# Kernel optimization log

Hardware: AMD Instinct MI355X
Metric: run time of the kernel (lower is better)

Reference implementation:

```python
import jax, jax.numpy as jnp
import numpy as np

N_NODES = 50000
N_EDGES = 1200000
D_FEAT = 64
HIDDEN = 32


def setup_inputs() -> dict:
    key = jax.random.key(0)
    ks = jax.random.split(key, 9)
    x = jax.random.normal(ks[0], (N_NODES, D_FEAT), dtype=jnp.float32)
    edge_index = jax.random.randint(ks[1], (2, N_EDGES), 0, N_NODES, dtype=jnp.int64)
    u = jax.random.normal(ks[2], (N_NODES,), dtype=jnp.float32)
    d_in = 2 * D_FEAT
    # MLP: Linear(d_in,H) -> relu -> Linear(H,H) -> relu -> Linear(H,1)
    W1 = jax.random.normal(ks[3], (d_in, HIDDEN), dtype=jnp.float32) / np.sqrt(d_in)
    b1 = jnp.zeros((HIDDEN,), dtype=jnp.float32)
    W2 = jax.random.normal(ks[4], (HIDDEN, HIDDEN), dtype=jnp.float32) / np.sqrt(HIDDEN)
    b2 = jnp.zeros((HIDDEN,), dtype=jnp.float32)
    W3 = jax.random.normal(ks[5], (HIDDEN, 1), dtype=jnp.float32) / np.sqrt(HIDDEN)
    b3 = jnp.zeros((1,), dtype=jnp.float32)
    return {"x": x, "edge_index": edge_index, "u": u,
            "W1": W1, "b1": b1, "W2": W2, "b2": b2, "W3": W3, "b3": b3}


def reference(x, edge_index, u, W1, b1, W2, b2, W3, b3):
    row, col = edge_index[0], edge_index[1]
    # gather + concat: [E, 2*D]
    x_edge = jnp.concatenate([x[row], x[col]], axis=-1)
    # per-edge MLP -> scalar weight per edge
    h = jax.nn.relu(x_edge @ W1 + b1)
    h = jax.nn.relu(h @ W2 + b2)
    edge_weight = (h @ W3 + b3)[:, 0]  # [E]
    # spmm: f[i] = sum_{e: row[e]==i} w_e * u[col[e]]
    f = jax.ops.segment_sum(edge_weight * u[col], row, num_segments=x.shape[0])
    return f
```

## Files before the change

kernel.cpp:

```cpp
#include <hip/hip_runtime.h>

#define N_NODES 50000
#define N_EDGES 1200000
#define N_TILES (N_NODES / 16)
#define W1T_STRIDE 72
#define K1_BLOCKS 782

#define N_BUCKETS 196
#define BUCKET_CAP 7168
#define CHUNKS_PER_WAVE 15
#define EDGES_PER_BLOCK 1920
#define KA_BLOCKS 625

typedef __attribute__((ext_vector_type(8))) short short8;
typedef __attribute__((ext_vector_type(4))) float floatx4;

__device__ __forceinline__ unsigned short f32_to_bf16(float f) {
    unsigned int v = __float_as_uint(f);
    unsigned int r = v + 0x7FFFu + ((v >> 16) & 1u);
    return (unsigned short)(r >> 16);
}
__device__ __forceinline__ float bf16_to_f32(unsigned short s) {
    return __uint_as_float(((unsigned int)s) << 16);
}
__device__ __forceinline__ unsigned int pack_bf16x2(float lo, float hi) {
    return (unsigned int)f32_to_bf16(lo) | ((unsigned int)f32_to_bf16(hi) << 16);
}

__global__ __launch_bounds__(256) void precompute_P_mfma(
    const float* __restrict__ x, const float* __restrict__ W1,
    const float* __restrict__ b1, unsigned short* __restrict__ P,
    int* __restrict__ cursor)
{
    const int tid  = threadIdx.x;
    const int gtid = blockIdx.x * 256 + tid;

    if (gtid < N_BUCKETS) cursor[gtid] = 0;

    __shared__ unsigned short W1t[64 * W1T_STRIDE];
    for (int e = tid; e < 128 * 32; e += 256) {
        const int kp = e >> 5, jp = e & 31;
        W1t[((kp < 64) ? jp : jp + 32) * W1T_STRIDE + (kp & 63)] =
            f32_to_bf16(W1[e]);
    }
    __syncthreads();

    const int lane = tid & 63;
    const int n = lane & 15;
    const int q = lane >> 4;

    const int tile = blockIdx.x * 4 + (tid >> 6);
    if (tile >= N_TILES) return;

    short8 bw[4][2];
    #pragma unroll
    for (int G = 0; G < 4; ++G)
        #pragma unroll
        for (int h = 0; h < 2; ++h)
            bw[G][h] = *(const short8*)
                &W1t[(n + 16 * G) * W1T_STRIDE + h * 32 + q * 8];
    const float bias0 = b1[n], bias1 = b1[n + 16];

    const int node = tile * 16 + n;
    const float4* xp  = (const float4*)(x + (size_t)node * 64 + q * 8);
    const float4 xa = xp[0], xb = xp[1];
    const float4* xp2 = (const float4*)(x + (size_t)node * 64 + 32 + q * 8);
    const float4 xc = xp2[0], xd = xp2[1];

    short8 a0, a1;
    a0[0] = (short)f32_to_bf16(xa.x); a0[1] = (short)f32_to_bf16(xa.y);
    a0[2] = (short)f32_to_bf16(xa.z); a0[3] = (short)f32_to_bf16(xa.w);
    a0[4] = (short)f32_to_bf16(xb.x); a0[5] = (short)f32_to_bf16(xb.y);
    a0[6] = (short)f32_to_bf16(xb.z); a0[7] = (short)f32_to_bf16(xb.w);
    a1[0] = (short)f32_to_bf16(xc.x); a1[1] = (short)f32_to_bf16(xc.y);
    a1[2] = (short)f32_to_bf16(xc.z); a1[3] = (short)f32_to_bf16(xc.w);
    a1[4] = (short)f32_to_bf16(xd.x); a1[5] = (short)f32_to_bf16(xd.y);
    a1[6] = (short)f32_to_bf16(xd.z); a1[7] = (short)f32_to_bf16(xd.w);

    unsigned int* P32 = (unsigned int*)P;
    floatx4 acc[4];
    #pragma unroll
    for (int G = 0; G < 4; ++G) {
        const float bi = (G == 0) ? bias0 : (G == 1) ? bias1 : 0.0f;
        acc[G] = (floatx4){bi, bi, bi, bi};
        acc[G] = __builtin_amdgcn_mfma_f32_16x16x32_bf16(a0, bw[G][0], acc[G], 0, 0, 0);
        acc[G] = __builtin_amdgcn_mfma_f32_16x16x32_bf16(a1, bw[G][1], acc[G], 0, 0, 0);
    }
    #pragma unroll
    for (int r = 0; r < 4; ++r) {
        const int nr = tile * 16 + q * 4 + r;
        P32[(size_t)nr * 32 + n]      = pack_bf16x2(acc[0][r], acc[1][r]);
        P32[(size_t)nr * 32 + 16 + n] = pack_bf16x2(acc[2][r], acc[3][r]);
    }
}

__global__ __launch_bounds__(256) void edge_mlp_bin(
    const int* __restrict__ row, const int* __restrict__ col,
    const float* __restrict__ u,
    const float* __restrict__ W2, const float* __restrict__ b2,
    const float* __restrict__ W3, const float* __restrict__ b3,
    const unsigned short* __restrict__ P,
    unsigned int* __restrict__ buf, int* __restrict__ cursor)
{
    __shared__ unsigned short rankv[EDGES_PER_BLOCK];
    __shared__ int hist[N_BUCKETS];
    __shared__ int base[N_BUCKETS];

    const int tid = threadIdx.x;
    for (int b = tid; b < N_BUCKETS; b += 256) hist[b] = 0;
    __syncthreads();

    const int blockStart = blockIdx.x * EDGES_PER_BLOCK;

    for (int i = tid; i < EDGES_PER_BLOCK; i += 256) {
        const int r = row[blockStart + i];
        rankv[i] = (unsigned short)atomicAdd(&hist[r >> 8], 1);
    }
    __syncthreads();

    for (int b = tid; b < N_BUCKETS; b += 256)
        base[b] = atomicAdd(&cursor[b], hist[b]);
    __syncthreads();

    const int lane = tid & 63;
    const int n = lane & 15;
    const int q = lane >> 4;
    const int wave = tid >> 6;

    short8 bf0, bf1;
    #pragma unroll
    for (int i = 0; i < 8; ++i) {
        const int F = q * 4 + (i >> 1) + 16 * (i & 1);
        bf0[i] = (short)f32_to_bf16(W2[F * 32 + n]);
        bf1[i] = (short)f32_to_bf16(W2[F * 32 + n + 16]);
    }
    const float w3n0 = W3[n], w3n1 = W3[n + 16];
    const float b2n0 = b2[n], b2n1 = b2[n + 16];
    const float bias3 = b3[0];

    #pragma unroll 1
    for (int ci = 0; ci < CHUNKS_PER_WAVE; ++ci) {
        const int cloc  = (wave * CHUNKS_PER_WAVE + ci) * 32;
        const int base0 = blockStart + cloc;

        int rI[2], cI[2];
        #pragma unroll
        for (int t = 0; t < 2; ++t) {
            const int e = base0 + t * 16 + n;
            rI[t] = row[e];
            cI[t] = col[e];
        }
        int r2 = 0, eloc = 0; float u2 = 0.0f;
        if (n < 8) {
            eloc = cloc + 16 * (n >> 2) + 4 * q + (n & 3);
            const int e2 = blockStart + eloc;
            r2 = row[e2];
            u2 = u[col[e2]];
        }
        short8 v1[2], v2[2];
        #pragma unroll
        for (int t = 0; t < 2; ++t) {
            v1[t] = *(const short8*)(P + (size_t)rI[t] * 64 + q * 8);
            v2[t] = *(const short8*)(P + (size_t)cI[t] * 64 + 32 + q * 8);
        }

        float tr[2][4];
        #pragma unroll
        for (int t = 0; t < 2; ++t) {
            short8 a;
            #pragma unroll
            for (int i = 0; i < 8; ++i) {
                const float f1 = bf16_to_f32((unsigned short)v1[t][i]);
                const float f2 = bf16_to_f32((unsigned short)v2[t][i]);
                a[i] = (short)f32_to_bf16(fmaxf(f1 + f2, 0.0f));
            }
            floatx4 d0 = {b2n0, b2n0, b2n0, b2n0};
            floatx4 d1 = {b2n1, b2n1, b2n1, b2n1};
            d0 = __builtin_amdgcn_mfma_f32_16x16x32_bf16(a, bf0, d0, 0, 0, 0);
            d1 = __builtin_amdgcn_mfma_f32_16x16x32_bf16(a, bf1, d1, 0, 0, 0);
            #pragma unroll
            for (int r = 0; r < 4; ++r)
                tr[t][r] = fmaxf(d0[r], 0.0f) * w3n0 + fmaxf(d1[r], 0.0f) * w3n1;
        }

        #pragma unroll
        for (int mask = 1; mask < 16; mask <<= 1) {
            #pragma unroll
            for (int t = 0; t < 2; ++t)
                #pragma unroll
                for (int r = 0; r < 4; ++r)
                    tr[t][r] += __shfl_xor(tr[t][r], mask, 64);
        }

        if (n < 8) {
            const float va0 = (n & 4) ? tr[1][0] : tr[0][0];
            const float va1 = (n & 4) ? tr[1][1] : tr[0][1];
            const float va2 = (n & 4) ? tr[1][2] : tr[0][2];
            const float va3 = (n & 4) ? tr[1][3] : tr[0][3];
            const float vb0 = (n & 2) ? va2 : va0;
            const float vb1 = (n & 2) ? va3 : va1;
            const float v   = (n & 1) ? vb1 : vb0;
            const float val = (v + bias3) * u2;

            const int bin  = r2 >> 8;
            const int slot = base[bin] + (int)rankv[eloc];
            buf[(size_t)bin * BUCKET_CAP + slot] =
                ((unsigned int)f32_to_bf16(val) << 16) | (unsigned int)(r2 & 255);
        }
    }
}

__global__ __launch_bounds__(256) void bucket_reduce(
    const unsigned int* __restrict__ buf, const int* __restrict__ cursor,
    float* __restrict__ out)
{
    __shared__ float acc[256];
    const int b   = blockIdx.x;
    const int tid = threadIdx.x;
    acc[tid] = 0.0f;
    __syncthreads();

    const int cnt = cursor[b];
    const unsigned int* bb = buf + (size_t)b * BUCKET_CAP;
    for (int i = tid; i < cnt; i += 256) {
        const unsigned int ent = bb[i];
        atomicAdd(&acc[ent & 255u],
                  bf16_to_f32((unsigned short)(ent >> 16)));
    }
    __syncthreads();

    const int node = b * 256 + tid;
    if (node < N_NODES) out[node] = acc[tid];
}

extern "C" void kernel_launch(void* const* d_in, const int* in_sizes, int n_in,
                              void* d_out, int out_size, void* d_ws, size_t ws_size,
                              hipStream_t stream)
{
    const float* x    = (const float*)d_in[0];
    const int*   eidx = (const int*)  d_in[1];
    const float* u    = (const float*)d_in[2];
    const float* W1   = (const float*)d_in[3];
    const float* b1   = (const float*)d_in[4];
    const float* W2   = (const float*)d_in[5];
    const float* b2   = (const float*)d_in[6];
    const float* W3   = (const float*)d_in[7];
    const float* b3   = (const float*)d_in[8];

    const int* row = eidx;
    const int* col = eidx + N_EDGES;

    unsigned short* P   = (unsigned short*)d_ws;
    unsigned int*   buf = (unsigned int*)((char*)d_ws + (size_t)N_NODES * 128);
    int* cursor = (int*)((char*)d_ws + (size_t)N_NODES * 128
                         + (size_t)N_BUCKETS * BUCKET_CAP * 4);
    float* out = (float*)d_out;

    precompute_P_mfma<<<K1_BLOCKS, 256, 0, stream>>>(x, W1, b1, P, cursor);

    edge_mlp_bin<<<KA_BLOCKS, 256, 0, stream>>>(
        row, col, u, W2, b2, W3, b3, P, buf, cursor);

    bucket_reduce<<<N_BUCKETS, 256, 0, stream>>>(buf, cursor, out);
}
```

Baseline: 150.2 us.

## Bin edges by destination first, then run edge MLP per bucket with shared-memory accumulation

The pipeline is reordered. Edges are first binned by row bucket, storing (local row, col) entries, and a per-bucket kernel then runs the MLP and accumulates directly into LDS before atomically adding to the output. The P table is split into row and col halves so row-side gathers stay within a bucket's compact 16KB slice, which should improve cache locality. The separate reduce kernel and the bf16 rounding of edge values are gone. In exchange, the output needs zero-initialisation and global atomics, and the work per bucket is uneven.

```diff
diff --git a/kernel.cpp b/kernel.cpp
--- a/kernel.cpp
+++ b/kernel.cpp
@@ -8,9 +8,9 @@
 
 #define N_BUCKETS 196
 #define BUCKET_CAP 7168
-#define CHUNKS_PER_WAVE 15
 #define EDGES_PER_BLOCK 1920
 #define KA_BLOCKS 625
+#define KB_SPLIT 4
 
 typedef __attribute__((ext_vector_type(8))) short short8;
 typedef __attribute__((ext_vector_type(4))) float floatx4;
@@ -29,13 +29,16 @@
 
 __global__ __launch_bounds__(256) void precompute_P_mfma(
     const float* __restrict__ x, const float* __restrict__ W1,
-    const float* __restrict__ b1, unsigned short* __restrict__ P,
-    int* __restrict__ cursor)
+    const float* __restrict__ b1,
+    unsigned short* __restrict__ P1, unsigned short* __restrict__ P2,
+    int* __restrict__ cursor, float* __restrict__ out)
 {
     const int tid  = threadIdx.x;
     const int gtid = blockIdx.x * 256 + tid;
 
     if (gtid < N_BUCKETS) cursor[gtid] = 0;
+    for (int i = gtid; i < N_NODES; i += K1_BLOCKS * 256)
+        out[i] = 0.0f;
 
     __shared__ unsigned short W1t[64 * W1T_STRIDE];
     for (int e = tid; e < 128 * 32; e += 256) {
@@ -77,7 +80,6 @@
     a1[4] = (short)f32_to_bf16(xd.x); a1[5] = (short)f32_to_bf16(xd.y);
     a1[6] = (short)f32_to_bf16(xd.z); a1[7] = (short)f32_to_bf16(xd.w);
 
-    unsigned int* P32 = (unsigned int*)P;
     floatx4 acc[4];
     #pragma unroll
     for (int G = 0; G < 4; ++G) {
@@ -86,41 +88,63 @@
         acc[G] = __builtin_amdgcn_mfma_f32_16x16x32_bf16(a0, bw[G][0], acc[G], 0, 0, 0);
         acc[G] = __builtin_amdgcn_mfma_f32_16x16x32_bf16(a1, bw[G][1], acc[G], 0, 0, 0);
     }
+    unsigned int* P1d = (unsigned int*)P1;
+    unsigned int* P2d = (unsigned int*)P2;
     #pragma unroll
     for (int r = 0; r < 4; ++r) {
         const int nr = tile * 16 + q * 4 + r;
-        P32[(size_t)nr * 32 + n]      = pack_bf16x2(acc[0][r], acc[1][r]);
-        P32[(size_t)nr * 32 + 16 + n] = pack_bf16x2(acc[2][r], acc[3][r]);
-    }
-}
-
-__global__ __launch_bounds__(256) void edge_mlp_bin(
+        P1d[(size_t)nr * 16 + n] = pack_bf16x2(acc[0][r], acc[1][r]);
+        P2d[(size_t)nr * 16 + n] = pack_bf16x2(acc[2][r], acc[3][r]);
+    }
+}
+
+__global__ __launch_bounds__(256) void edge_bin(
     const int* __restrict__ row, const int* __restrict__ col,
+    unsigned int* __restrict__ buf, int* __restrict__ cursor)
+{
+    __shared__ unsigned short rankv[EDGES_PER_BLOCK];
+    __shared__ int hist[N_BUCKETS];
+    __shared__ int base[N_BUCKETS];
+
+    const int tid = threadIdx.x;
+    for (int b = tid; b < N_BUCKETS; b += 256) hist[b] = 0;
+    __syncthreads();
+
+    const int blockStart = blockIdx.x * EDGES_PER_BLOCK;
+
+    for (int i = tid; i < EDGES_PER_BLOCK; i += 256) {
+        const int r = row[blockStart + i];
+        rankv[i] = (unsigned short)atomicAdd(&hist[r >> 8], 1);
+    }
+    __syncthreads();
+
+    for (int b = tid; b < N_BUCKETS; b += 256)
+        base[b] = atomicAdd(&cursor[b], hist[b]);
+    __syncthreads();
+
+    for (int i = tid; i < EDGES_PER_BLOCK; i += 256) {
+        const int r = row[blockStart + i];
+        const int c = col[blockStart + i];
+        const int bin = r >> 8;
+        buf[(size_t)bin * BUCKET_CAP + base[bin] + (int)rankv[i]] =
+            ((unsigned int)(r & 255) << 24) | (unsigned int)c;
+    }
+}
+
+__global__ __launch_bounds__(256) void bucket_mlp(
     const float* __restrict__ u,
     const float* __restrict__ W2, const float* __restrict__ b2,
     const float* __restrict__ W3, const float* __restrict__ b3,
-    const unsigned short* __restrict__ P,
-    unsigned int* __restrict__ buf, int* __restrict__ cursor)
-{
-    __shared__ unsigned short rankv[EDGES_PER_BLOCK];
-    __shared__ int hist[N_BUCKETS];
-    __shared__ int base[N_BUCKETS];
-
+    const unsigned short* __restrict__ P1, const unsigned short* __restrict__ P2,
+    const unsigned int* __restrict__ buf, const int* __restrict__ cursor,
+    float* __restrict__ out)
+{
+    __shared__ float accs[256];
     const int tid = threadIdx.x;
-    for (int b = tid; b < N_BUCKETS; b += 256) hist[b] = 0;
-    __syncthreads();
-
-    const int blockStart = blockIdx.x * EDGES_PER_BLOCK;
-
-    for (int i = tid; i < EDGES_PER_BLOCK; i += 256) {
-        const int r = row[blockStart + i];
-        rankv[i] = (unsigned short)atomicAdd(&hist[r >> 8], 1);
-    }
-    __syncthreads();
-
-    for (int b = tid; b < N_BUCKETS; b += 256)
-        base[b] = atomicAdd(&cursor[b], hist[b]);
-    __syncthreads();
+    accs[tid] = 0.0f;
+
+    const int b = blockIdx.x >> 2;
+    const int s = blockIdx.x & (KB_SPLIT - 1);
 
     const int lane = tid & 63;
     const int n = lane & 15;
@@ -138,30 +162,38 @@
     const float b2n0 = b2[n], b2n1 = b2[n + 16];
     const float bias3 = b3[0];
 
+    __syncthreads();
+
+    const int cnt = cursor[b];
+    const unsigned int* bb = buf + (size_t)b * BUCKET_CAP;
+    const unsigned short* P1b = P1 + (size_t)b * 256 * 32;
+    const int nch = (cnt + 31) >> 5;
+
     #pragma unroll 1
-    for (int ci = 0; ci < CHUNKS_PER_WAVE; ++ci) {
-        const int cloc  = (wave * CHUNKS_PER_WAVE + ci) * 32;
-        const int base0 = blockStart + cloc;
-
-        int rI[2], cI[2];
+    for (int ch = s * 4 + wave; ch < nch; ch += KB_SPLIT * 4) {
+        const int base0 = ch * 32;
+
+        int rl[2], cI[2];
         #pragma unroll
         for (int t = 0; t < 2; ++t) {
-            const int e = base0 + t * 16 + n;
-            rI[t] = row[e];
-            cI[t] = col[e];
-        }
-        int r2 = 0, eloc = 0; float u2 = 0.0f;
+            int e = base0 + t * 16 + n;
+            if (e >= cnt) e = cnt - 1;
+            const unsigned int ent = bb[e];
+            rl[t] = (int)(ent >> 24);
+            cI[t] = (int)(ent & 0x1FFFFu);
+        }
+        int r2 = 0; float u2 = 0.0f;
         if (n < 8) {
-            eloc = cloc + 16 * (n >> 2) + 4 * q + (n & 3);
-            const int e2 = blockStart + eloc;
-            r2 = row[e2];
-            u2 = u[col[e2]];
+            const int eloc = base0 + 16 * (n >> 2) + 4 * q + (n & 3);
+            const unsigned int ent2 = bb[(eloc < cnt) ? eloc : 0];
+            r2 = (int)(ent2 >> 24);
+            u2 = (eloc < cnt) ? u[ent2 & 0x1FFFFu] : 0.0f;
         }
         short8 v1[2], v2[2];
         #pragma unroll
         for (int t = 0; t < 2; ++t) {
-            v1[t] = *(const short8*)(P + (size_t)rI[t] * 64 + q * 8);
-            v2[t] = *(const short8*)(P + (size_t)cI[t] * 64 + 32 + q * 8);
+            v1[t] = *(const short8*)(P1b + (size_t)rl[t] * 32 + q * 8);
+            v2[t] = *(const short8*)(P2 + (size_t)cI[t] * 32 + q * 8);
         }
 
         float tr[2][4];
@@ -200,37 +232,17 @@
             const float vb0 = (n & 2) ? va2 : va0;
             const float vb1 = (n & 2) ? va3 : va1;
             const float v   = (n & 1) ? vb1 : vb0;
-            const float val = (v + bias3) * u2;
-
-            const int bin  = r2 >> 8;
-            const int slot = base[bin] + (int)rankv[eloc];
-            buf[(size_t)bin * BUCKET_CAP + slot] =
-                ((unsigned int)f32_to_bf16(val) << 16) | (unsigned int)(r2 & 255);
-        }
-    }
-}
-
-__global__ __launch_bounds__(256) void bucket_reduce(
-    const unsigned int* __restrict__ buf, const int* __restrict__ cursor,
-    float* __restrict__ out)
-{
-    __shared__ float acc[256];
-    const int b   = blockIdx.x;
-    const int tid = threadIdx.x;
-    acc[tid] = 0.0f;
-    __syncthreads();
-
-    const int cnt = cursor[b];
-    const unsigned int* bb = buf + (size_t)b * BUCKET_CAP;
-    for (int i = tid; i < cnt; i += 256) {
-        const unsigned int ent = bb[i];
-        atomicAdd(&acc[ent & 255u],
-                  bf16_to_f32((unsigned short)(ent >> 16)));
-    }
+            atomicAdd(&accs[r2], (v + bias3) * u2);
+        }
+    }
+
     __syncthreads();
 
     const int node = b * 256 + tid;
-    if (node < N_NODES) out[node] = acc[tid];
+    if (node < N_NODES) {
+        const float val = accs[tid];
+        atomicAdd(out + node, val);
+    }
 }
 
 extern "C" void kernel_launch(void* const* d_in, const int* in_sizes, int n_in,
@@ -250,16 +262,17 @@
     const int* row = eidx;
     const int* col = eidx + N_EDGES;
 
-    unsigned short* P   = (unsigned short*)d_ws;
-    unsigned int*   buf = (unsigned int*)((char*)d_ws + (size_t)N_NODES * 128);
+    unsigned short* P1 = (unsigned short*)d_ws;
+    unsigned short* P2 = (unsigned short*)((char*)d_ws + (size_t)N_NODES * 64);
+    unsigned int*  buf = (unsigned int*)((char*)d_ws + (size_t)N_NODES * 128);
     int* cursor = (int*)((char*)d_ws + (size_t)N_NODES * 128
                          + (size_t)N_BUCKETS * BUCKET_CAP * 4);
     float* out = (float*)d_out;
 
-    precompute_P_mfma<<<K1_BLOCKS, 256, 0, stream>>>(x, W1, b1, P, cursor);
-
-    edge_mlp_bin<<<KA_BLOCKS, 256, 0, stream>>>(
-        row, col, u, W2, b2, W3, b3, P, buf, cursor);
-
-    bucket_reduce<<<N_BUCKETS, 256, 0, stream>>>(buf, cursor, out);
-}
+    precompute_P_mfma<<<K1_BLOCKS, 256, 0, stream>>>(x, W1, b1, P1, P2, cursor, out);
+
+    edge_bin<<<KA_BLOCKS, 256, 0, stream>>>(row, col, buf, cursor);
+
+    bucket_mlp<<<N_BUCKETS * KB_SPLIT, 256, 0, stream>>>(
+        u, W2, b2, W3, b3, P1, P2, buf, cursor, out);
+}
```

Measured after the change: 138.5 us. -7.8%, faster.
